# Optimization experiments

Measured on AMD Instinct MI355X. Metric: run time of the kernel, lower is better.

The kernel has to match this reference:

```python
import jax, jax.numpy as jnp
import numpy as np

NUM_HEADS = 16
HEAD_DIM = 128
Q_SCALE = 0.05
Q_ZP = 8.0


def _quant_dequant_int4(x, scale, zp):
    # simulate int4 pack/unpack: q = clamp(round(x/scale + zp), 0, 15); deq = (q - zp) * scale
    qv = jnp.clip(jnp.round(x / scale + zp), 0.0, 15.0)
    return (qv - zp) * scale


def setup_inputs() -> dict:
    key = jax.random.key(0)
    kq, kk, kv = jax.random.split(key, 3)
    B, Sq, Sk, D = 4, 2048, 2048, 2048
    q = jax.random.normal(kq, (B, Sq, D), dtype=jnp.float32)
    k = jax.random.normal(kk, (B, Sk, D), dtype=jnp.float32)
    v = jax.random.normal(kv, (B, Sk, D), dtype=jnp.float32)
    mask = jnp.ones((B, Sk), dtype=bool)
    return {"q": q, "k": k, "v": v, "mask": mask, "q_start": 1000000000}


def reference(q, k, v, mask, q_start):
    B, Sq, d_model = q.shape
    Sk = k.shape[1]
    H, Dh = NUM_HEADS, HEAD_DIM
    # [B, H, S, Dh]
    qh = q.reshape(B, Sq, H, Dh).transpose(0, 2, 1, 3)
    kh = k.reshape(B, Sk, H, Dh).transpose(0, 2, 1, 3)
    vh = v.reshape(B, Sk, H, Dh).transpose(0, 2, 1, 3)
    # int4 quant-dequant of K and V (per-tensor scale/zero-point path)
    kd = _quant_dequant_int4(kh, Q_SCALE, Q_ZP)
    vd = _quant_dequant_int4(vh, Q_SCALE, Q_ZP)
    inv_sqrt_d = 1.0 / np.sqrt(Dh).astype(np.float32)
    scores = jnp.einsum('bhmd,bhnd->bhmn', qh, kd) * inv_sqrt_d  # [B,H,Sq,Sk]
    neg_inf = jnp.finfo(scores.dtype).min
    # key padding mask [B, Sk]
    scores = jnp.where(mask[:, None, None, :], scores, neg_inf)
    # causal mask with absolute query offset q_start (disabled when q_start is huge)
    m_abs = q_start + jnp.arange(Sq)[:, None]  # absolute query positions
    n_pos = jnp.arange(Sk)[None, :]
    scores = jnp.where(n_pos <= m_abs, scores, neg_inf)
    attn = jax.nn.softmax(scores, axis=-1)
    out = jnp.einsum('bhmn,bhnd->bhmd', attn, vd)  # [B,H,Sq,Dh]
    return out.transpose(0, 2, 1, 3).reshape(B, Sq, d_model)
```

## Files before the change

kernel.cpp:

```cpp
#include <hip/hip_runtime.h>


typedef __attribute__((ext_vector_type(8))) short short8;
typedef __attribute__((ext_vector_type(16))) float f32x16;

#define DEVI __device__ __forceinline__

namespace {

constexpr int DM = 2048;
constexpr int SQ = 2048;
constexpr int SK = 2048;
constexpr int DH = 128;
constexpr int KVB = 32;
constexpr int NT = SK / KVB;
constexpr int TILE_E = KVB * DH;
constexpr float CEXP = 0.12752051393f;
constexpr float DEFER = 62.0f;

union US8 { unsigned short u[8]; short8 v; };
union UP4 { unsigned int u[4]; short8 v; };

DEVI unsigned short f2bf(float f) {
  unsigned int u = __float_as_uint(f);
  return (unsigned short)((u + 0x7fffu + ((u >> 16) & 1u)) >> 16);
}

DEVI float dq(float x) {
  float t = __builtin_rintf(__builtin_fmaf(x, 20.0f, 8.0f));
  t = __builtin_fmaxf(t, 0.0f);
  t = __builtin_fminf(t, 15.0f);
  return (t - 8.0f) * 0.05f;
}

DEVI unsigned short dqb(float x) { return f2bf(dq(x)); }

}

__global__ __launch_bounds__(512)
void eit3_pre(const float* __restrict__ kg, const float* __restrict__ vg,
              unsigned short* __restrict__ kws, unsigned short* __restrict__ vws)
{
  const int tid = threadIdx.x;
  const int t = blockIdx.x, h = blockIdx.y, b = blockIdx.z;
  const size_t tb = (((size_t)(b * 16 + h)) * NT + t) * TILE_E;
  __shared__ __align__(16) unsigned short VL[32 * 132];

  {
    const int g = tid;
    const int n = g >> 4;
    const int dsw = ((g & 15) * 8) ^ ((n & 7) << 3);
    const float* src = kg + ((size_t)b * SK + (size_t)t * KVB + n) * DM + h * DH + dsw;
    float4 fa = *(const float4*)src;
    float4 fb = *(const float4*)(src + 4);
    US8 o;
    o.u[0] = dqb(fa.x); o.u[1] = dqb(fa.y); o.u[2] = dqb(fa.z); o.u[3] = dqb(fa.w);
    o.u[4] = dqb(fb.x); o.u[5] = dqb(fb.y); o.u[6] = dqb(fb.z); o.u[7] = dqb(fb.w);
    *(short8*)(kws + tb + (size_t)g * 8) = o.v;
  }
  {
    const int r = tid >> 4, dg = tid & 15;
    const float* src = vg + ((size_t)b * SK + (size_t)t * KVB + r) * DM + h * DH + dg * 8;
    float4 fa = *(const float4*)src;
    float4 fb = *(const float4*)(src + 4);
    US8 o;
    o.u[0] = dqb(fa.x); o.u[1] = dqb(fa.y); o.u[2] = dqb(fa.z); o.u[3] = dqb(fa.w);
    o.u[4] = dqb(fb.x); o.u[5] = dqb(fb.y); o.u[6] = dqb(fb.z); o.u[7] = dqb(fb.w);
    *(short8*)(VL + r * 132 + (dg ^ ((r >> 3) & 3)) * 8) = o.v;
  }
  __syncthreads();
  {
    const int g2 = tid;
    const int d = g2 >> 2;
    const int kgr = (g2 & 3) ^ ((d >> 1) & 3);
    US8 o;
#pragma unroll
    for (int i = 0; i < 8; ++i) {
      int r = kgr * 8 + i;
      o.u[i] = VL[r * 132 + (d ^ (kgr * 8))];
    }
    *(short8*)(vws + tb + (size_t)g2 * 8) = o.v;
  }
}

__global__ __launch_bounds__(256, 2)
void eit3_attn(const unsigned short* __restrict__ kws,
               const unsigned short* __restrict__ vws,
               const float* __restrict__ qg,
               const unsigned char* __restrict__ maskg,
               const int* __restrict__ qsg, float* __restrict__ outg)
{
  const int tid  = threadIdx.x;
  const int lane = tid & 63;
  const int w    = tid >> 6;
  const int hi   = lane >> 5;
  const int ql   = lane & 31;
  const int hi8  = hi * 8;
  const int phys = blockIdx.x;
  const int xcd = phys & 7, slot = phys >> 3;
  const int bh = 8 * (slot >> 4) + xcd;
  const int qb = slot & 15;
  const int h = bh & 15, b = bh >> 4;
  const int q0 = qb * 128;
  const long long qstart = (long long)qsg[0];

  __shared__ __align__(16) unsigned short Ksh[2][TILE_E];
  __shared__ __align__(16) unsigned short Vsh[2][TILE_E];
  __shared__ unsigned char mskSh[2][32];

  const unsigned char* mrow = maskg + (size_t)b * SK;
  int ok_u8, ok_i32;
  {
    const unsigned int* p = (const unsigned int*)(mrow + tid * 8);
    unsigned int w0 = p[0], w1 = p[1];
    int a0 = (w0 & 0xFFu) && (w0 & 0xFF00u) && (w0 & 0xFF0000u) && (w0 & 0xFF000000u);
    int a1 = (w1 & 0xFFu) && (w1 & 0xFF00u) && (w1 & 0xFF0000u) && (w1 & 0xFF000000u);
    ok_u8  = a0 && a1;
    ok_i32 = (w0 == 1u) && (w1 == 1u);
  }
  const int a_u8  = __syncthreads_and(ok_u8);
  const int a_i32 = __syncthreads_and(ok_i32);
  const bool mask_all = (a_u8 | a_i32) != 0;

  const size_t tbase = (size_t)bh * NT * TILE_E;

  auto stage = [&](int buf, int t) {
    const unsigned short* kt = kws + tbase + (size_t)t * TILE_E + w * 1024 + lane * 8;
    const unsigned short* vt = vws + tbase + (size_t)t * TILE_E + w * 1024 + lane * 8;
    char* kd = (char*)&Ksh[0][0] + buf * 8192 + w * 2048;
    char* vd = (char*)&Vsh[0][0] + buf * 8192 + w * 2048;
    __builtin_amdgcn_global_load_lds(
        (const __attribute__((address_space(1))) void*)kt,
        (__attribute__((address_space(3))) void*)kd, 16, 0, 0);
    __builtin_amdgcn_global_load_lds(
        (const __attribute__((address_space(1))) void*)(kt + 512),
        (__attribute__((address_space(3))) void*)(kd + 1024), 16, 0, 0);
    __builtin_amdgcn_global_load_lds(
        (const __attribute__((address_space(1))) void*)vt,
        (__attribute__((address_space(3))) void*)vd, 16, 0, 0);
    __builtin_amdgcn_global_load_lds(
        (const __attribute__((address_space(1))) void*)(vt + 512),
        (__attribute__((address_space(3))) void*)(vd + 1024), 16, 0, 0);
  };

  stage(0, 0);

  short8 qf[8];
  {
    const float* qp = qg + ((size_t)b * SQ + q0 + w * 32 + ql) * DM + h * DH + hi8;
#pragma unroll
    for (int s = 0; s < 8; ++s) {
      float4 fa = *(const float4*)(qp + s * 16);
      float4 fb = *(const float4*)(qp + s * 16 + 4);
      US8 t;
      t.u[0] = f2bf(fa.x); t.u[1] = f2bf(fa.y); t.u[2] = f2bf(fa.z); t.u[3] = f2bf(fa.w);
      t.u[4] = f2bf(fb.x); t.u[5] = f2bf(fb.y); t.u[6] = f2bf(fb.z); t.u[7] = f2bf(fb.w);
      qf[s] = t.v;
    }
  }

  f32x16 zv;
#pragma unroll
  for (int r = 0; r < 16; ++r) zv[r] = 0.0f;
  f32x16 acc[4];
  acc[0] = zv; acc[1] = zv; acc[2] = zv; acc[3] = zv;
  float M = -3.0e38f, L = 0.0f;
  const long long qlim = qstart + (long long)(q0 + w * 32 + ql);

  {
    bool f0 = mask_all && ((long long)(KVB - 1) <= qstart + (long long)q0);
    if (!f0 && w == 0 && lane < 32) mskSh[0][lane] = mrow[lane];
  }
  __syncthreads();

  int cur = 0;
  for (int ti = 0; ti < NT; ++ti) {
    const int kv0 = ti * KVB;
    const int nxt = cur ^ 1;
    if (ti + 1 < NT) {
      stage(nxt, ti + 1);
      bool fn = mask_all && ((long long)(kv0 + 2 * KVB - 1) <= qstart + (long long)q0);
      if (!fn && w == 0 && lane < 32) mskSh[nxt][lane] = mrow[kv0 + KVB + lane];
    }
    const bool fast = mask_all && ((long long)(kv0 + KVB - 1) <= qstart + (long long)q0);

    const unsigned short* Kc = &Ksh[cur][0];
    const unsigned short* Vc = &Vsh[cur][0];

    f32x16 st = zv;
    __builtin_amdgcn_s_setprio(1);
#pragma unroll
    for (int s = 0; s < 8; ++s) {
      short8 af = *(const short8*)(Kc + ql * 128 + ((s * 16 + hi8) ^ ((ql & 7) << 3)));
      st = __builtin_amdgcn_mfma_f32_32x32x16_bf16(af, qf[s], st, 0, 0, 0);
    }
    __builtin_amdgcn_s_setprio(0);

    if (!fast) {
#pragma unroll
      for (int r = 0; r < 16; ++r) {
        int nl = (r & 3) + 8 * (r >> 2) + 4 * hi;
        bool ok = (mskSh[cur][nl] != 0) && ((long long)(kv0 + nl) <= qlim);
        if (!ok) st[r] = -3.0e38f;
      }
    }

    float t8[8];
#pragma unroll
    for (int i = 0; i < 8; ++i) t8[i] = __builtin_fmaxf(st[i], st[i + 8]);
#pragma unroll
    for (int i = 0; i < 4; ++i) t8[i] = __builtin_fmaxf(t8[i], t8[i + 4]);
    float pmax = __builtin_fmaxf(__builtin_fmaxf(t8[0], t8[1]),
                                 __builtin_fmaxf(t8[2], t8[3]));
    pmax = __builtin_fmaxf(pmax, __shfl_xor(pmax, 32));
    if (!__all(pmax <= M + DEFER)) {
      float Mn = __builtin_fmaxf(M, pmax);
      float sc = __builtin_amdgcn_exp2f((M - Mn) * CEXP);
      L *= sc;
#pragma unroll
      for (int r = 0; r < 16; ++r) {
        float s2 = __shfl(sc, (r & 3) + 8 * (r >> 2) + 4 * hi);
        acc[0][r] *= s2; acc[1][r] *= s2; acc[2][r] *= s2; acc[3][r] *= s2;
      }
      M = Mn;
    }
#pragma unroll
    for (int r = 0; r < 16; ++r)
      st[r] = __builtin_amdgcn_exp2f((st[r] - M) * CEXP);
    if (!fast) {
#pragma unroll
      for (int r = 0; r < 16; ++r) {
        int nl = (r & 3) + 8 * (r >> 2) + 4 * hi;
        bool ok = (mskSh[cur][nl] != 0) && ((long long)(kv0 + nl) <= qlim);
        if (!ok) st[r] = 0.0f;
      }
    }
    float s8[8];
#pragma unroll
    for (int i = 0; i < 8; ++i) s8[i] = st[i] + st[i + 8];
#pragma unroll
    for (int i = 0; i < 4; ++i) s8[i] = s8[i] + s8[i + 4];
    float ps = (s8[0] + s8[1]) + (s8[2] + s8[3]);
    ps += __shfl_xor(ps, 32);
    L += ps;

    short8 pa[2];
#pragma unroll
    for (int ks = 0; ks < 2; ++ks) {
      const int m8 = ks * 8;
      unsigned int X0, X1, Y0, Y1;
      asm("v_cvt_pk_bf16_f32 %0, %1, %2" : "=v"(X0) : "v"(st[m8 + 0]), "v"(st[m8 + 1]));
      asm("v_cvt_pk_bf16_f32 %0, %1, %2" : "=v"(X1) : "v"(st[m8 + 2]), "v"(st[m8 + 3]));
      asm("v_cvt_pk_bf16_f32 %0, %1, %2" : "=v"(Y0) : "v"(st[m8 + 4]), "v"(st[m8 + 5]));
      asm("v_cvt_pk_bf16_f32 %0, %1, %2" : "=v"(Y1) : "v"(st[m8 + 6]), "v"(st[m8 + 7]));
      asm("v_permlane32_swap_b32 %0, %1" : "+v"(X0), "+v"(Y0));
      asm("v_permlane32_swap_b32 %0, %1" : "+v"(X1), "+v"(Y1));
      UP4 P;
      P.u[0] = X0; P.u[1] = X1; P.u[2] = Y0; P.u[3] = Y1;
      pa[ks] = P.v;
    }

    __builtin_amdgcn_s_setprio(1);
#pragma unroll
    for (int n = 0; n < 4; ++n) {
      const unsigned short* vrow = Vc + n * 1024 + ql * 32;
#pragma unroll
      for (int ks = 0; ks < 2; ++ks) {
        short8 vb = *(const short8*)(vrow + ((ks * 16 + hi8) ^ (((ql >> 1) & 3) << 3)));
        acc[n] = __builtin_amdgcn_mfma_f32_32x32x16_bf16(pa[ks], vb, acc[n], 0, 0, 0);
      }
    }
    __builtin_amdgcn_s_setprio(0);

    __syncthreads();
    cur = nxt;
  }

  if (L == 0.0f) L = 1.0f;
  float rinv = 1.0f / L;
#pragma unroll
  for (int r = 0; r < 16; ++r) {
    int cr = (r & 3) + 8 * (r >> 2) + 4 * hi;
    float inv = __shfl(rinv, cr);
    float* op = outg + ((size_t)b * SQ + q0 + w * 32 + cr) * DM + h * DH + ql;
    op[0]  = acc[0][r] * inv;
    op[32] = acc[1][r] * inv;
    op[64] = acc[2][r] * inv;
    op[96] = acc[3][r] * inv;
  }
}

__global__ __launch_bounds__(512, 2)
void eit3_attn_fb(const float* __restrict__ qg, const float* __restrict__ kg,
                  const float* __restrict__ vg, const unsigned char* __restrict__ maskg,
                  const int* __restrict__ qsg, float* __restrict__ outg)
{
  const int tid  = threadIdx.x;
  const int lane = tid & 63;
  const int w    = tid >> 6;
  const int hi   = lane >> 5;
  const int ql   = lane & 31;
  const int qb = blockIdx.x;
  const int h  = blockIdx.y;
  const int b  = blockIdx.z;
  const int q0 = qb * 256;
  const long long qstart = (long long)qsg[0];

  __shared__ __align__(16) unsigned short Ksh[64 * 128];
  __shared__ __align__(16) unsigned short Vsh[64 * 128];
  __shared__ unsigned char mskSh[64];

  const unsigned int vbase = (unsigned int)(size_t)(void*)Vsh;

  const unsigned char* mrow = maskg + (size_t)b * SK;
  int ok_u8, ok_i32;
  {
    const unsigned char* p4 = mrow + tid * 4;
    unsigned char b0 = p4[0], b1 = p4[1], b2 = p4[2], b3 = p4[3];
    ok_u8  = (b0 && b1 && b2 && b3);
    ok_i32 = (b0 && !b1 && !b2 && !b3);
  }
  const int a_u8  = __syncthreads_and(ok_u8);
  const int a_i32 = __syncthreads_and(ok_i32);
  const bool mask_all = (a_u8 | a_i32) != 0;

  short8 qf[8];
  {
    const int qrow = q0 + w * 32 + ql;
    const float* qp = qg + ((size_t)b * SQ + qrow) * DM + h * DH + hi * 8;
#pragma unroll
    for (int s = 0; s < 8; ++s) {
      float4 fa = *(const float4*)(qp + s * 16);
      float4 fb = *(const float4*)(qp + s * 16 + 4);
      US8 t;
      t.u[0] = f2bf(fa.x); t.u[1] = f2bf(fa.y); t.u[2] = f2bf(fa.z); t.u[3] = f2bf(fa.w);
      t.u[4] = f2bf(fb.x); t.u[5] = f2bf(fb.y); t.u[6] = f2bf(fb.z); t.u[7] = f2bf(fb.w);
      qf[s] = t.v;
    }
  }

  f32x16 zv;
#pragma unroll
  for (int r = 0; r < 16; ++r) zv[r] = 0.0f;
  f32x16 acc[4];
  acc[0] = zv; acc[1] = zv; acc[2] = zv; acc[3] = zv;
  float M = -3.0e38f, L = 0.0f;

  const float* kptr = kg + ((size_t)b * SK) * DM + h * DH;
  const float* vptr = vg + ((size_t)b * SK) * DM + h * DH;

  for (int kv0 = 0; kv0 < SK; kv0 += 64) {
    __syncthreads();
#pragma unroll
    for (int j = 0; j < 2; ++j) {
      int idx = tid + 512 * j;
      int n = idx >> 4, d8 = idx & 15;
      const float* gp = kptr + (size_t)(kv0 + n) * DM + d8 * 8;
      float4 fa = *(const float4*)gp;
      float4 fb = *(const float4*)(gp + 4);
      US8 t;
      t.u[0] = dqb(fa.x); t.u[1] = dqb(fa.y); t.u[2] = dqb(fa.z); t.u[3] = dqb(fa.w);
      t.u[4] = dqb(fb.x); t.u[5] = dqb(fb.y); t.u[6] = dqb(fb.z); t.u[7] = dqb(fb.w);
      int ui = (n * 128 + d8 * 8) ^ ((n & 7) << 3);
      *(short8*)(Ksh + ui) = t.v;
    }
    {
      int kr = w * 8 + (lane & 7);
      int c3 = lane >> 3;
#pragma unroll
      for (int j = 0; j < 4; ++j) {
        int d4 = c3 + 8 * j;
        const float* gp = vptr + (size_t)(kv0 + kr) * DM + d4 * 4;
        float4 fa = *(const float4*)gp;
        ushort4 tv;
        tv.x = dqb(fa.x); tv.y = dqb(fa.y); tv.z = dqb(fa.z); tv.w = dqb(fa.w);
        int d = d4 * 4;
        int ui = ((kr >> 2) * 8 + (d >> 4)) * 64 + (kr & 3) * 16 + (d & 15);
        *(ushort4*)(Vsh + ui) = tv;
      }
    }
    const bool causal_ok = ((long long)kv0 + 63) <= (qstart + (long long)q0);
    const bool fast = mask_all && causal_ok;
    if (!fast && w == 0) mskSh[lane] = mrow[kv0 + lane];
    __syncthreads();

    f32x16 st[2];
#pragma unroll
    for (int t = 0; t < 2; ++t) {
      f32x16 sa = zv;
#pragma unroll
      for (int s = 0; s < 8; ++s) {
        int kr = t * 32 + ql;
        int ui = (kr * 128 + s * 16 + hi * 8) ^ ((kr & 7) << 3);
        short8 af = *(const short8*)(Ksh + ui);
        sa = __builtin_amdgcn_mfma_f32_32x32x16_bf16(af, qf[s], sa, 0, 0, 0);
      }
      st[t] = sa;
    }
    if (!fast) {
      const long long qlim = qstart + (long long)(q0 + w * 32 + ql);
#pragma unroll
      for (int t = 0; t < 2; ++t) {
#pragma unroll
        for (int r = 0; r < 16; ++r) {
          int nl = t * 32 + (r & 3) + 8 * (r >> 2) + 4 * hi;
          bool ok = (mskSh[nl] != 0) && ((long long)(kv0 + nl) <= qlim);
          if (!ok) st[t][r] = -3.0e38f;
        }
      }
    }
    f32x16 red;
#pragma unroll
    for (int r = 0; r < 16; ++r) red[r] = __builtin_fmaxf(st[0][r], st[1][r]);
#pragma unroll
    for (int r = 0; r < 8; ++r) red[r] = __builtin_fmaxf(red[r], red[r + 8]);
#pragma unroll
    for (int r = 0; r < 4; ++r) red[r] = __builtin_fmaxf(red[r], red[r + 4]);
    float pmax = __builtin_fmaxf(__builtin_fmaxf(red[0], red[1]),
                                 __builtin_fmaxf(red[2], red[3]));
    pmax = __builtin_fmaxf(pmax, __shfl_xor(pmax, 32));
    const float Mnew = __builtin_fmaxf(M, pmax);
    const float scale = __builtin_amdgcn_exp2f((M - Mnew) * CEXP);
#pragma unroll
    for (int t = 0; t < 2; ++t) {
#pragma unroll
      for (int r = 0; r < 16; ++r)
        st[t][r] = __builtin_amdgcn_exp2f((st[t][r] - Mnew) * CEXP);
    }
    if (!fast) {
      const long long qlim = qstart + (long long)(q0 + w * 32 + ql);
#pragma unroll
      for (int t = 0; t < 2; ++t) {
#pragma unroll
        for (int r = 0; r < 16; ++r) {
          int nl = t * 32 + (r & 3) + 8 * (r >> 2) + 4 * hi;
          bool ok = (mskSh[nl] != 0) && ((long long)(kv0 + nl) <= qlim);
          if (!ok) st[t][r] = 0.0f;
        }
      }
    }
    f32x16 sx;
#pragma unroll
    for (int r = 0; r < 16; ++r) sx[r] = st[0][r] + st[1][r];
#pragma unroll
    for (int r = 0; r < 8; ++r) sx[r] = sx[r] + sx[r + 8];
#pragma unroll
    for (int r = 0; r < 4; ++r) sx[r] = sx[r] + sx[r + 4];
    float ps = (sx[0] + sx[1]) + (sx[2] + sx[3]);
    ps += __shfl_xor(ps, 32);
    L = L * scale + ps;
    if (!__all(Mnew == M)) {
#pragma unroll
      for (int r = 0; r < 16; ++r) {
        float sc = __shfl(scale, (r & 3) + 8 * (r >> 2) + 4 * hi);
        acc[0][r] *= sc; acc[1][r] *= sc; acc[2][r] *= sc; acc[3][r] *= sc;
      }
    }
    M = Mnew;

    short8 pa[4];
#pragma unroll
    for (int ks = 0; ks < 4; ++ks) {
      const int t = ks >> 1;
      const int m8 = (ks & 1) * 8;
      unsigned int X0, X1, Y0, Y1;
      asm("v_cvt_pk_bf16_f32 %0, %1, %2" : "=v"(X0) : "v"(st[t][m8 + 0]), "v"(st[t][m8 + 1]));
      asm("v_cvt_pk_bf16_f32 %0, %1, %2" : "=v"(X1) : "v"(st[t][m8 + 2]), "v"(st[t][m8 + 3]));
      asm("v_cvt_pk_bf16_f32 %0, %1, %2" : "=v"(Y0) : "v"(st[t][m8 + 4]), "v"(st[t][m8 + 5]));
      asm("v_cvt_pk_bf16_f32 %0, %1, %2" : "=v"(Y1) : "v"(st[t][m8 + 6]), "v"(st[t][m8 + 7]));
      asm("v_permlane32_swap_b32 %0, %1" : "+v"(X0), "+v"(Y0));
      asm("v_permlane32_swap_b32 %0, %1" : "+v"(X1), "+v"(Y1));
      UP4 P;
      P.u[0] = X0; P.u[1] = X1; P.u[2] = Y0; P.u[3] = Y1;
      pa[ks] = P.v;
    }
#pragma unroll
    for (int n = 0; n < 4; ++n) {
      unsigned long long t0[4], t1[4];
#pragma unroll
      for (int ks = 0; ks < 4; ++ks) {
        unsigned int addr = vbase
          + (unsigned int)(((4 * ks + 2 * hi) * 8 + 2 * n + ((lane >> 4) & 1)) * 128)
          + (unsigned int)((lane & 15) * 8);
        asm volatile("ds_read_b64_tr_b16 %0, %1" : "=v"(t0[ks]) : "v"(addr));
        asm volatile("ds_read_b64_tr_b16 %0, %1 offset:1024" : "=v"(t1[ks]) : "v"(addr));
      }
      asm volatile("s_waitcnt lgkmcnt(0)" ::: "memory");
      __builtin_amdgcn_sched_barrier(0);
#pragma unroll
      for (int ks = 0; ks < 4; ++ks) {
        union { unsigned long long q[2]; short8 v; } vb;
        vb.q[0] = t0[ks]; vb.q[1] = t1[ks];
        acc[n] = __builtin_amdgcn_mfma_f32_32x32x16_bf16(pa[ks], vb.v, acc[n], 0, 0, 0);
      }
    }
  }

  if (L == 0.0f) L = 1.0f;
  float rinv = 1.0f / L;
#pragma unroll
  for (int r = 0; r < 16; ++r) {
    int cr = (r & 3) + 8 * (r >> 2) + 4 * hi;
    float inv = __shfl(rinv, cr);
    float* op = outg + ((size_t)b * SQ + (q0 + w * 32 + cr)) * DM + h * DH + ql;
    op[0]  = acc[0][r] * inv;
    op[32] = acc[1][r] * inv;
    op[64] = acc[2][r] * inv;
    op[96] = acc[3][r] * inv;
  }
}

extern "C" void kernel_launch(void* const* d_in, const int* in_sizes, int n_in,
                              void* d_out, int out_size, void* d_ws, size_t ws_size,
                              hipStream_t stream) {
  (void)in_sizes; (void)n_in; (void)out_size;
  const float* q = (const float*)d_in[0];
  const float* k = (const float*)d_in[1];
  const float* v = (const float*)d_in[2];
  const unsigned char* mask = (const unsigned char*)d_in[3];
  const int* qs = (const int*)d_in[4];

  const size_t need = (size_t)2 * 16777216 * 2;
  if (ws_size >= need) {
    unsigned short* kws = (unsigned short*)d_ws;
    unsigned short* vws = kws + 16777216;
    dim3 pgrid(NT, 16, 4);
    eit3_pre<<<pgrid, dim3(512), 0, stream>>>(k, v, kws, vws);
    eit3_attn<<<dim3(1024), dim3(256), 0, stream>>>(kws, vws, q, mask, qs, (float*)d_out);
  } else {
    dim3 grid(SQ / 256, 16, 4);
    eit3_attn_fb<<<grid, dim3(512), 0, stream>>>(q, k, v, mask, qs, (float*)d_out);
  }
}
```

Measured before the change: 229.4 us.

## Triple-buffer K/V tiles and issue next QK^T ahead of current softmax

Grows the LDS K/V/mask ring from two to three buffers and prefetches two tiles ahead. The loop is restructured so the QK^T MFMAs for tile t+1 are issued before the softmax and PV work of tile t. Two score accumulators alternate, and the loop is unrolled by two with rotating buffer indices. The goal is to overlap matrix-core work with the exp/max/sum VALU phase and hide more load latency. In exchange it uses more LDS and more VGPRs for the extra score tile, and it drops the priority hints around the QK^T block.

Result: faster. 220.6 us (-3.8%).

```diff
diff --git a/kernel.cpp b/kernel.cpp
--- a/kernel.cpp
+++ b/kernel.cpp
@@ -104,9 +104,9 @@
   const int q0 = qb * 128;
   const long long qstart = (long long)qsg[0];
 
-  __shared__ __align__(16) unsigned short Ksh[2][TILE_E];
-  __shared__ __align__(16) unsigned short Vsh[2][TILE_E];
-  __shared__ unsigned char mskSh[2][32];
+  __shared__ __align__(16) unsigned short Ksh[3][TILE_E];
+  __shared__ __align__(16) unsigned short Vsh[3][TILE_E];
+  __shared__ unsigned char mskSh[3][32];
 
   const unsigned char* mrow = maskg + (size_t)b * SK;
   int ok_u8, ok_i32;
@@ -144,6 +144,7 @@
   };
 
   stage(0, 0);
+  stage(1, 1);
 
   short8 qf[8];
   {
@@ -167,47 +168,50 @@
   float M = -3.0e38f, L = 0.0f;
   const long long qlim = qstart + (long long)(q0 + w * 32 + ql);
 
+  auto qkt = [&](const unsigned short* Kc, f32x16& out) {
+    f32x16 sa = zv;
+#pragma unroll
+    for (int s = 0; s < 8; ++s) {
+      short8 af = *(const short8*)(Kc + ql * 128 + ((s * 16 + hi8) ^ ((ql & 7) << 3)));
+      sa = __builtin_amdgcn_mfma_f32_32x32x16_bf16(af, qf[s], sa, 0, 0, 0);
+    }
+    out = sa;
+  };
+
   {
     bool f0 = mask_all && ((long long)(KVB - 1) <= qstart + (long long)q0);
     if (!f0 && w == 0 && lane < 32) mskSh[0][lane] = mrow[lane];
+    bool f1 = mask_all && ((long long)(2 * KVB - 1) <= qstart + (long long)q0);
+    if (!f1 && w == 0 && lane < 32) mskSh[1][lane] = mrow[KVB + lane];
   }
   __syncthreads();
 
-  int cur = 0;
-  for (int ti = 0; ti < NT; ++ti) {
-    const int kv0 = ti * KVB;
-    const int nxt = cur ^ 1;
-    if (ti + 1 < NT) {
-      stage(nxt, ti + 1);
-      bool fn = mask_all && ((long long)(kv0 + 2 * KVB - 1) <= qstart + (long long)q0);
-      if (!fn && w == 0 && lane < 32) mskSh[nxt][lane] = mrow[kv0 + KVB + lane];
-    }
+  f32x16 stA, stB;
+  qkt(&Ksh[0][0], stA);
+
+  auto step = [&](int t, f32x16& stP, f32x16& stN, int b0, int b1, int b2) {
+    const int kv0 = t * KVB;
+    if (t + 2 < NT) {
+      stage(b2, t + 2);
+      bool fn = mask_all && ((long long)(kv0 + 3 * KVB - 1) <= qstart + (long long)q0);
+      if (!fn && w == 0 && lane < 32) mskSh[b2][lane] = mrow[kv0 + 2 * KVB + lane];
+    }
+    if (t + 1 < NT) qkt(&Ksh[b1][0], stN);
+
     const bool fast = mask_all && ((long long)(kv0 + KVB - 1) <= qstart + (long long)q0);
-
-    const unsigned short* Kc = &Ksh[cur][0];
-    const unsigned short* Vc = &Vsh[cur][0];
-
-    f32x16 st = zv;
-    __builtin_amdgcn_s_setprio(1);
-#pragma unroll
-    for (int s = 0; s < 8; ++s) {
-      short8 af = *(const short8*)(Kc + ql * 128 + ((s * 16 + hi8) ^ ((ql & 7) << 3)));
-      st = __builtin_amdgcn_mfma_f32_32x32x16_bf16(af, qf[s], st, 0, 0, 0);
-    }
-    __builtin_amdgcn_s_setprio(0);
 
     if (!fast) {
 #pragma unroll
       for (int r = 0; r < 16; ++r) {
         int nl = (r & 3) + 8 * (r >> 2) + 4 * hi;
-        bool ok = (mskSh[cur][nl] != 0) && ((long long)(kv0 + nl) <= qlim);
-        if (!ok) st[r] = -3.0e38f;
+        bool ok = (mskSh[b0][nl] != 0) && ((long long)(kv0 + nl) <= qlim);
+        if (!ok) stP[r] = -3.0e38f;
       }
     }
 
     float t8[8];
 #pragma unroll
-    for (int i = 0; i < 8; ++i) t8[i] = __builtin_fmaxf(st[i], st[i + 8]);
+    for (int i = 0; i < 8; ++i) t8[i] = __builtin_fmaxf(stP[i], stP[i + 8]);
 #pragma unroll
     for (int i = 0; i < 4; ++i) t8[i] = __builtin_fmaxf(t8[i], t8[i + 4]);
     float pmax = __builtin_fmaxf(__builtin_fmaxf(t8[0], t8[1]),
@@ -226,18 +230,18 @@
     }
 #pragma unroll
     for (int r = 0; r < 16; ++r)
-      st[r] = __builtin_amdgcn_exp2f((st[r] - M) * CEXP);
+      stP[r] = __builtin_amdgcn_exp2f((stP[r] - M) * CEXP);
     if (!fast) {
 #pragma unroll
       for (int r = 0; r < 16; ++r) {
         int nl = (r & 3) + 8 * (r >> 2) + 4 * hi;
-        bool ok = (mskSh[cur][nl] != 0) && ((long long)(kv0 + nl) <= qlim);
-        if (!ok) st[r] = 0.0f;
+        bool ok = (mskSh[b0][nl] != 0) && ((long long)(kv0 + nl) <= qlim);
+        if (!ok) stP[r] = 0.0f;
       }
     }
     float s8[8];
 #pragma unroll
-    for (int i = 0; i < 8; ++i) s8[i] = st[i] + st[i + 8];
+    for (int i = 0; i < 8; ++i) s8[i] = stP[i] + stP[i + 8];
 #pragma unroll
     for (int i = 0; i < 4; ++i) s8[i] = s8[i] + s8[i + 4];
     float ps = (s8[0] + s8[1]) + (s8[2] + s8[3]);
@@ -249,10 +253,10 @@
     for (int ks = 0; ks < 2; ++ks) {
       const int m8 = ks * 8;
       unsigned int X0, X1, Y0, Y1;
-      asm("v_cvt_pk_bf16_f32 %0, %1, %2" : "=v"(X0) : "v"(st[m8 + 0]), "v"(st[m8 + 1]));
-      asm("v_cvt_pk_bf16_f32 %0, %1, %2" : "=v"(X1) : "v"(st[m8 + 2]), "v"(st[m8 + 3]));
-      asm("v_cvt_pk_bf16_f32 %0, %1, %2" : "=v"(Y0) : "v"(st[m8 + 4]), "v"(st[m8 + 5]));
-      asm("v_cvt_pk_bf16_f32 %0, %1, %2" : "=v"(Y1) : "v"(st[m8 + 6]), "v"(st[m8 + 7]));
+      asm("v_cvt_pk_bf16_f32 %0, %1, %2" : "=v"(X0) : "v"(stP[m8 + 0]), "v"(stP[m8 + 1]));
+      asm("v_cvt_pk_bf16_f32 %0, %1, %2" : "=v"(X1) : "v"(stP[m8 + 2]), "v"(stP[m8 + 3]));
+      asm("v_cvt_pk_bf16_f32 %0, %1, %2" : "=v"(Y0) : "v"(stP[m8 + 4]), "v"(stP[m8 + 5]));
+      asm("v_cvt_pk_bf16_f32 %0, %1, %2" : "=v"(Y1) : "v"(stP[m8 + 6]), "v"(stP[m8 + 7]));
       asm("v_permlane32_swap_b32 %0, %1" : "+v"(X0), "+v"(Y0));
       asm("v_permlane32_swap_b32 %0, %1" : "+v"(X1), "+v"(Y1));
       UP4 P;
@@ -260,6 +264,7 @@
       pa[ks] = P.v;
     }
 
+    const unsigned short* Vc = &Vsh[b0][0];
     __builtin_amdgcn_s_setprio(1);
 #pragma unroll
     for (int n = 0; n < 4; ++n) {
@@ -273,7 +278,13 @@
     __builtin_amdgcn_s_setprio(0);
 
     __syncthreads();
-    cur = nxt;
+  };
+
+  int bA = 0, bB = 1, bC = 2;
+  for (int t = 0; t < NT; t += 2) {
+    step(t,     stA, stB, bA, bB, bC);
+    step(t + 1, stB, stA, bB, bC, bA);
+    int tmp = bA; bA = bC; bC = bB; bB = tmp;
   }
 
   if (L == 0.0f) L = 1.0f;
```

## Pre-swizzle K/V into MFMA fragment order and load directly to registers

Applied to the files above, without the earlier changes.

The preprocessing kernel now writes dequantized K and V tiles in exactly the per-lane MFMA fragment layout. This lets the attention kernel load fragments straight from global memory into registers, with no LDS staging, no per-tile __syncthreads and no shared mask buffer. K fragments are double-buffered in registers across an unrolled pair of steps, and the mask is read directly from global memory when needed. This removes LDS traffic and block-wide barriers, but it raises register pressure and exposes global-load latency, because each V load sits right before its use.

Measured after the change: 220.9 us. 3.7% less time.

```diff
diff --git a/kernel.cpp b/kernel.cpp
--- a/kernel.cpp
+++ b/kernel.cpp
@@ -44,42 +44,39 @@
   const int tid = threadIdx.x;
   const int t = blockIdx.x, h = blockIdx.y, b = blockIdx.z;
   const size_t tb = (((size_t)(b * 16 + h)) * NT + t) * TILE_E;
-  __shared__ __align__(16) unsigned short VL[32 * 132];
-
-  {
-    const int g = tid;
-    const int n = g >> 4;
-    const int dsw = ((g & 15) * 8) ^ ((n & 7) << 3);
-    const float* src = kg + ((size_t)b * SK + (size_t)t * KVB + n) * DM + h * DH + dsw;
-    float4 fa = *(const float4*)src;
-    float4 fb = *(const float4*)(src + 4);
+  __shared__ __align__(16) unsigned short KL[32 * 136];
+  __shared__ __align__(16) unsigned short VL[32 * 136];
+
+  {
+    const int r = tid >> 4, c8 = (tid & 15) * 8;
+    const float* ks = kg + ((size_t)b * SK + (size_t)t * KVB + r) * DM + h * DH + c8;
+    const float* vs = vg + ((size_t)b * SK + (size_t)t * KVB + r) * DM + h * DH + c8;
+    float4 ka = *(const float4*)ks, kb4 = *(const float4*)(ks + 4);
+    float4 va = *(const float4*)vs, vb4 = *(const float4*)(vs + 4);
+    US8 ok, ov;
+    ok.u[0] = dqb(ka.x); ok.u[1] = dqb(ka.y); ok.u[2] = dqb(ka.z); ok.u[3] = dqb(ka.w);
+    ok.u[4] = dqb(kb4.x); ok.u[5] = dqb(kb4.y); ok.u[6] = dqb(kb4.z); ok.u[7] = dqb(kb4.w);
+    ov.u[0] = dqb(va.x); ov.u[1] = dqb(va.y); ov.u[2] = dqb(va.z); ov.u[3] = dqb(va.w);
+    ov.u[4] = dqb(vb4.x); ov.u[5] = dqb(vb4.y); ov.u[6] = dqb(vb4.z); ov.u[7] = dqb(vb4.w);
+    *(short8*)(KL + r * 136 + c8) = ok.v;
+    *(short8*)(VL + r * 136 + c8) = ov.v;
+  }
+  __syncthreads();
+
+  const int l = tid & 63;
+  const int lq = l & 31, lh = (l >> 5) * 8;
+  {
+    const int s = tid >> 6;
+    short8 o = *(const short8*)(KL + lq * 136 + s * 16 + lh);
+    *(short8*)(kws + tb + (size_t)tid * 8) = o;
+  }
+  {
+    const int f = tid >> 6, n = f >> 1, ks2 = f & 1;
     US8 o;
-    o.u[0] = dqb(fa.x); o.u[1] = dqb(fa.y); o.u[2] = dqb(fa.z); o.u[3] = dqb(fa.w);
-    o.u[4] = dqb(fb.x); o.u[5] = dqb(fb.y); o.u[6] = dqb(fb.z); o.u[7] = dqb(fb.w);
-    *(short8*)(kws + tb + (size_t)g * 8) = o.v;
-  }
-  {
-    const int r = tid >> 4, dg = tid & 15;
-    const float* src = vg + ((size_t)b * SK + (size_t)t * KVB + r) * DM + h * DH + dg * 8;
-    float4 fa = *(const float4*)src;
-    float4 fb = *(const float4*)(src + 4);
-    US8 o;
-    o.u[0] = dqb(fa.x); o.u[1] = dqb(fa.y); o.u[2] = dqb(fa.z); o.u[3] = dqb(fa.w);
-    o.u[4] = dqb(fb.x); o.u[5] = dqb(fb.y); o.u[6] = dqb(fb.z); o.u[7] = dqb(fb.w);
-    *(short8*)(VL + r * 132 + (dg ^ ((r >> 3) & 3)) * 8) = o.v;
-  }
-  __syncthreads();
-  {
-    const int g2 = tid;
-    const int d = g2 >> 2;
-    const int kgr = (g2 & 3) ^ ((d >> 1) & 3);
-    US8 o;
-#pragma unroll
-    for (int i = 0; i < 8; ++i) {
-      int r = kgr * 8 + i;
-      o.u[i] = VL[r * 132 + (d ^ (kgr * 8))];
-    }
-    *(short8*)(vws + tb + (size_t)g2 * 8) = o.v;
+#pragma unroll
+    for (int j = 0; j < 8; ++j)
+      o.u[j] = VL[(ks2 * 16 + lh + j) * 136 + n * 32 + lq];
+    *(short8*)(vws + tb + (size_t)tid * 8) = o.v;
   }
 }
 
@@ -104,10 +101,6 @@
   const int q0 = qb * 128;
   const long long qstart = (long long)qsg[0];
 
-  __shared__ __align__(16) unsigned short Ksh[2][TILE_E];
-  __shared__ __align__(16) unsigned short Vsh[2][TILE_E];
-  __shared__ unsigned char mskSh[2][32];
-
   const unsigned char* mrow = maskg + (size_t)b * SK;
   int ok_u8, ok_i32;
   {
@@ -123,27 +116,8 @@
   const bool mask_all = (a_u8 | a_i32) != 0;
 
   const size_t tbase = (size_t)bh * NT * TILE_E;
-
-  auto stage = [&](int buf, int t) {
-    const unsigned short* kt = kws + tbase + (size_t)t * TILE_E + w * 1024 + lane * 8;
-    const unsigned short* vt = vws + tbase + (size_t)t * TILE_E + w * 1024 + lane * 8;
-    char* kd = (char*)&Ksh[0][0] + buf * 8192 + w * 2048;
-    char* vd = (char*)&Vsh[0][0] + buf * 8192 + w * 2048;
-    __builtin_amdgcn_global_load_lds(
-        (const __attribute__((address_space(1))) void*)kt,
-        (__attribute__((address_space(3))) void*)kd, 16, 0, 0);
-    __builtin_amdgcn_global_load_lds(
-        (const __attribute__((address_space(1))) void*)(kt + 512),
-        (__attribute__((address_space(3))) void*)(kd + 1024), 16, 0, 0);
-    __builtin_amdgcn_global_load_lds(
-        (const __attribute__((address_space(1))) void*)vt,
-        (__attribute__((address_space(3))) void*)vd, 16, 0, 0);
-    __builtin_amdgcn_global_load_lds(
-        (const __attribute__((address_space(1))) void*)(vt + 512),
-        (__attribute__((address_space(3))) void*)(vd + 1024), 16, 0, 0);
-  };
-
-  stage(0, 0);
+  const unsigned short* kb = kws + tbase + lane * 8;
+  const unsigned short* vb = vws + tbase + lane * 8;
 
   short8 qf[8];
   {
@@ -167,40 +141,43 @@
   float M = -3.0e38f, L = 0.0f;
   const long long qlim = qstart + (long long)(q0 + w * 32 + ql);
 
-  {
-    bool f0 = mask_all && ((long long)(KVB - 1) <= qstart + (long long)q0);
-    if (!f0 && w == 0 && lane < 32) mskSh[0][lane] = mrow[lane];
-  }
-  __syncthreads();
-
-  int cur = 0;
-  for (int ti = 0; ti < NT; ++ti) {
-    const int kv0 = ti * KVB;
-    const int nxt = cur ^ 1;
-    if (ti + 1 < NT) {
-      stage(nxt, ti + 1);
-      bool fn = mask_all && ((long long)(kv0 + 2 * KVB - 1) <= qstart + (long long)q0);
-      if (!fn && w == 0 && lane < 32) mskSh[nxt][lane] = mrow[kv0 + KVB + lane];
-    }
-    const bool fast = mask_all && ((long long)(kv0 + KVB - 1) <= qstart + (long long)q0);
-
-    const unsigned short* Kc = &Ksh[cur][0];
-    const unsigned short* Vc = &Vsh[cur][0];
+  short8 kfA[8], kfB[8];
+  {
+#pragma unroll
+    for (int s = 0; s < 8; ++s) kfA[s] = *(const short8*)(kb + s * 512);
+  }
+
+  auto step = [&](int t, short8 (&kfP)[8], short8 (&kfN)[8]) {
+    const int kv0 = t * KVB;
+
+    short8 vf[8];
+    {
+      const unsigned short* p = vb + (size_t)t * TILE_E;
+#pragma unroll
+      for (int f = 0; f < 8; ++f) vf[f] = *(const short8*)(p + f * 512);
+    }
 
     f32x16 st = zv;
     __builtin_amdgcn_s_setprio(1);
 #pragma unroll
-    for (int s = 0; s < 8; ++s) {
-      short8 af = *(const short8*)(Kc + ql * 128 + ((s * 16 + hi8) ^ ((ql & 7) << 3)));
-      st = __builtin_amdgcn_mfma_f32_32x32x16_bf16(af, qf[s], st, 0, 0, 0);
-    }
+    for (int s = 0; s < 8; ++s)
+      st = __builtin_amdgcn_mfma_f32_32x32x16_bf16(kfP[s], qf[s], st, 0, 0, 0);
     __builtin_amdgcn_s_setprio(0);
+
+    {
+      const int tn = (t + 1 < NT) ? (t + 1) : (NT - 1);
+      const unsigned short* p = kb + (size_t)tn * TILE_E;
+#pragma unroll
+      for (int s = 0; s < 8; ++s) kfN[s] = *(const short8*)(p + s * 512);
+    }
+
+    const bool fast = mask_all && ((long long)(kv0 + KVB - 1) <= qstart + (long long)q0);
 
     if (!fast) {
 #pragma unroll
       for (int r = 0; r < 16; ++r) {
         int nl = (r & 3) + 8 * (r >> 2) + 4 * hi;
-        bool ok = (mskSh[cur][nl] != 0) && ((long long)(kv0 + nl) <= qlim);
+        bool ok = (mrow[kv0 + nl] != 0) && ((long long)(kv0 + nl) <= qlim);
         if (!ok) st[r] = -3.0e38f;
       }
     }
@@ -231,7 +208,7 @@
 #pragma unroll
       for (int r = 0; r < 16; ++r) {
         int nl = (r & 3) + 8 * (r >> 2) + 4 * hi;
-        bool ok = (mskSh[cur][nl] != 0) && ((long long)(kv0 + nl) <= qlim);
+        bool ok = (mrow[kv0 + nl] != 0) && ((long long)(kv0 + nl) <= qlim);
         if (!ok) st[r] = 0.0f;
       }
     }
@@ -263,17 +240,17 @@
     __builtin_amdgcn_s_setprio(1);
 #pragma unroll
     for (int n = 0; n < 4; ++n) {
-      const unsigned short* vrow = Vc + n * 1024 + ql * 32;
-#pragma unroll
-      for (int ks = 0; ks < 2; ++ks) {
-        short8 vb = *(const short8*)(vrow + ((ks * 16 + hi8) ^ (((ql >> 1) & 3) << 3)));
-        acc[n] = __builtin_amdgcn_mfma_f32_32x32x16_bf16(pa[ks], vb, acc[n], 0, 0, 0);
-      }
+#pragma unroll
+      for (int ks = 0; ks < 2; ++ks)
+        acc[n] = __builtin_amdgcn_mfma_f32_32x32x16_bf16(pa[ks], vf[n * 2 + ks],
+                                                         acc[n], 0, 0, 0);
     }
     __builtin_amdgcn_s_setprio(0);
-
-    __syncthreads();
-    cur = nxt;
+  };
+
+  for (int t = 0; t < NT; t += 2) {
+    step(t, kfA, kfB);
+    step(t + 1, kfB, kfA);
   }
 
   if (L == 0.0f) L = 1.0f;
@@ -489,9 +466,9 @@
       __builtin_amdgcn_sched_barrier(0);
 #pragma unroll
       for (int ks = 0; ks < 4; ++ks) {
-        union { unsigned long long q[2]; short8 v; } vb;
-        vb.q[0] = t0[ks]; vb.q[1] = t1[ks];
-        acc[n] = __builtin_amdgcn_mfma_f32_32x32x16_bf16(pa[ks], vb.v, acc[n], 0, 0, 0);
+        union { unsigned long long q[2]; short8 v; } vb2;
+        vb2.q[0] = t0[ks]; vb2.q[1] = t1[ks];
+        acc[n] = __builtin_amdgcn_mfma_f32_32x32x16_bf16(pa[ks], vb2.v, acc[n], 0, 0, 0);
       }
     }
   }
```
